# Kernel tuning notes

Measured on AMD Instinct MI355X. Metric: run time of the kernel, lower is better.

## Reference

```python
import jax, jax.numpy as jnp
import numpy as np

PAD_ID = 0
N_LAYERS = 2


def setup_inputs() -> dict:
    key = jax.random.key(0)
    ks = jax.random.split(key, 10)
    B, T, S, H, V = 32, 64, 128, 512, 32000
    G = 4 * H
    sc = 0.02
    return {
        "context": jax.random.normal(ks[0], (B, S, H), jnp.float32),
        "dec_input": jax.random.randint(ks[1], (B, T), 0, V, jnp.int64),
        "h0": jnp.zeros((N_LAYERS, B, H), jnp.float32),
        "c0": jnp.zeros((N_LAYERS, B, H), jnp.float32),
        "emb_table": jax.random.normal(ks[2], (V, H), jnp.float32) * sc,
        "W_ih": jax.random.normal(ks[3], (N_LAYERS, G, H), jnp.float32) * sc,
        "W_hh": jax.random.normal(ks[4], (N_LAYERS, G, H), jnp.float32) * sc,
        "b_ih": jax.random.normal(ks[5], (N_LAYERS, G), jnp.float32) * sc,
        "b_hh": jax.random.normal(ks[6], (N_LAYERS, G), jnp.float32) * sc,
        "Wc": jax.random.normal(ks[7], (V, H), jnp.float32) * sc,
        "bc": jax.random.normal(ks[8], (V,), jnp.float32) * sc,
    }


def _lstm_cell(x, h, c, Wih, Whh, bih, bhh):
    # torch LSTMCell: gates in order i, f, g, o
    gates = x @ Wih.T + bih + h @ Whh.T + bhh  # [B, 4H]
    i, f, g, o = jnp.split(gates, 4, axis=-1)
    c_new = jax.nn.sigmoid(f) * c + jax.nn.sigmoid(i) * jnp.tanh(g)
    h_new = jax.nn.sigmoid(o) * jnp.tanh(c_new)
    return h_new, c_new


def _decode(context, dec_input, h0, c0, emb_table, W_ih, W_hh, b_ih, b_hh, Wc, bc):
    # padding_idx: embedding row pad_id is zero (and receives no grad)
    emb_table = emb_table.at[PAD_ID].set(0.0)
    embedded = emb_table[dec_input]           # [B, T, E]
    xs = jnp.swapaxes(embedded, 0, 1)         # [T, B, E]

    def step(carry, x_t):
        h, c = carry                          # each [L, B, H]
        inp = x_t
        new_h, new_c = [], []
        for l in range(N_LAYERS):
            h_new, c_new = _lstm_cell(inp, h[l], c[l], W_ih[l], W_hh[l], b_ih[l], b_hh[l])
            out = h_new
            # residual (dims match since embedding_dim == rnn_dim)
            inp = out + inp if inp.shape[-1] == out.shape[-1] else out
            new_h.append(h_new)
            new_c.append(c_new)
        # dot attention: score = bmm(context, target) -> [B, S]
        score = jnp.einsum('bsh,bh->bs', context, inp)
        log_attn = jax.nn.log_softmax(score, axis=1)
        # faithful to source: context weighted by LOG-softmax, summed over S
        ctx_vec = jnp.sum(context * log_attn[..., None], axis=1)  # [B, H]
        return (jnp.stack(new_h), jnp.stack(new_c)), ctx_vec

    (hT, cT), outs = jax.lax.scan(step, (h0, c0), xs)  # outs: [T, B, H]
    outs = jnp.swapaxes(outs, 0, 1)                    # [B, T, H]
    logits = outs @ Wc.T + bc                          # [B, T, V]
    return logits, hT, cT


def reference(context, dec_input, h0, c0, emb_table, W_ih, W_hh, b_ih, b_hh, Wc, bc):
    return _decode(context, dec_input, h0, c0, emb_table, W_ih, W_hh, b_ih, b_hh, Wc, bc)
```

## Files before the change

kernel.cpp:

```cpp
#include <hip/hip_runtime.h>
#include <hip/hip_bf16.h>

#define B_ 32
#define T_ 64
#define S_ 128
#define H_ 512
#define V_ 32000
#define G_ 2048
#define NBLK 128

typedef __bf16 bf16x8 __attribute__((ext_vector_type(8)));
typedef float  f32x4  __attribute__((ext_vector_type(4)));

__device__ __forceinline__ int frag_idx(int k, int b) {
    return ((((b >> 4) * 16 + (k >> 5)) * 4 + ((k >> 3) & 3)) * 16 + (b & 15)) * 8 + (k & 7);
}

__device__ __forceinline__ float sigm(float x) { return 1.f / (1.f + expf(-x)); }

__global__ __launch_bounds__(256) void k_embed(const int* __restrict__ dec,
                                               const float* __restrict__ emb,
                                               float* __restrict__ X,
                                               __hip_bfloat16* __restrict__ xfrag)
{
    int i   = blockIdx.x * 256 + threadIdx.x;
    int row = i >> 7;
    int b   = row >> 6, t = row & 63;
    int c4  = (i & 127) << 2;
    int tok = dec[row];
    float4 v = make_float4(0.f, 0.f, 0.f, 0.f);
    if (tok != 0) v = *(const float4*)(emb + (size_t)tok * H_ + c4);
    *(float4*)(X + (size_t)row * H_ + c4) = v;
    __hip_bfloat16* xf = xfrag + (size_t)t * (H_ * B_);
    xf[frag_idx(c4 + 0, b)] = __float2bfloat16(v.x);
    xf[frag_idx(c4 + 1, b)] = __float2bfloat16(v.y);
    xf[frag_idx(c4 + 2, b)] = __float2bfloat16(v.z);
    xf[frag_idx(c4 + 3, b)] = __float2bfloat16(v.w);
}

__global__ __launch_bounds__(256) void k_f2bf(const float* __restrict__ in,
                                              __hip_bfloat16* __restrict__ out, int n4)
{
    int i = blockIdx.x * 256 + threadIdx.x;
    if (i >= n4) return;
    float4 v = *(const float4*)(in + (size_t)i * 4);
    __hip_bfloat16* o = out + (size_t)i * 4;
    o[0] = __float2bfloat16(v.x); o[1] = __float2bfloat16(v.y);
    o[2] = __float2bfloat16(v.z); o[3] = __float2bfloat16(v.w);
}

__global__ __launch_bounds__(256, 1) void k_recur(
    const float* __restrict__ W_ih, const float* __restrict__ W_hh,
    const float* __restrict__ b_ih, const float* __restrict__ b_hh,
    const float* __restrict__ h0_in, const float* __restrict__ c0_in,
    const float* __restrict__ X, const __hip_bfloat16* __restrict__ xfrag,
    __hip_bfloat16* __restrict__ h0f, __hip_bfloat16* __restrict__ h1f,
    __hip_bfloat16* __restrict__ i1f,
    float* __restrict__ outs, float* __restrict__ out_states,
    unsigned* __restrict__ bar)
{
    __shared__ float red[2][4][2][16][17];
    const int tid  = threadIdx.x;
    const int blk  = blockIdx.x;
    const int lane = tid & 63;
    const int w    = tid >> 6;
    const int r    = lane & 15, lg = lane >> 4;

    const int q = r >> 2, jl = r & 3;
    const int g = q * 512 + blk * 4 + jl;
    const float* Wm[4] = { W_ih, W_hh, W_ih + (size_t)G_ * H_, W_hh + (size_t)G_ * H_ };
    bf16x8 wf[4][4];
#pragma unroll
    for (int m = 0; m < 4; m++)
#pragma unroll
        for (int s = 0; s < 4; s++) {
            const float* src = Wm[m] + (size_t)g * H_ + w * 128 + s * 32 + lg * 8;
            union { bf16x8 v; __hip_bfloat16 h[8]; } u;
#pragma unroll
            for (int e = 0; e < 8; e++) u.h[e] = __float2bfloat16(src[e]);
            wf[m][s] = u.v;
        }

    const int b = tid & 31, pjl = (tid >> 5) & 3, pj = blk * 4 + pjl;
    float c0r = 0.f, c1r = 0.f, i1r = 0.f, h0l = 0.f, h1l = 0.f;
    float b0r[4], b1r[4];
    if (tid < 128) {
        c0r = c0_in[b * H_ + pj];
        c1r = c0_in[B_ * H_ + b * H_ + pj];
#pragma unroll
        for (int qq = 0; qq < 4; qq++) {
            b0r[qq] = b_ih[qq * 512 + pj] + b_hh[qq * 512 + pj];
            b1r[qq] = b_ih[G_ + qq * 512 + pj] + b_hh[G_ + qq * 512 + pj];
        }
        h0f[0 * 16384 + frag_idx(pj, b)] = __float2bfloat16(h0_in[b * H_ + pj]);
        h1f[1 * 16384 + frag_idx(pj, b)] = __float2bfloat16(h0_in[B_ * H_ + b * H_ + pj]);
    }

    auto gbar = [&](int idx) {
        __syncthreads();
        if (tid == 0) {
            __threadfence();
            __hip_atomic_fetch_add(bar, 1u, __ATOMIC_RELEASE, __HIP_MEMORY_SCOPE_AGENT);
            unsigned tgt = (unsigned)NBLK * (unsigned)(idx + 1);
            while (__hip_atomic_load(bar, __ATOMIC_ACQUIRE, __HIP_MEMORY_SCOPE_AGENT) < tgt)
                __builtin_amdgcn_s_sleep(8);
            __threadfence();
        }
        __syncthreads();
    };

    gbar(0);

    for (int p = 0; p <= 64; ++p) {
        f32x4 acc0[2] = {}, acc1[2] = {};
        if (p <= 63) {
            const __hip_bfloat16* xb = xfrag + (size_t)p * 16384;
            const __hip_bfloat16* hb = h0f + (size_t)(p & 1) * 16384;
#pragma unroll
            for (int nt = 0; nt < 2; nt++)
#pragma unroll
                for (int s = 0; s < 4; s++) {
                    int ei = frag_idx(w * 128 + s * 32 + lg * 8, nt * 16 + r);
                    bf16x8 bx = *(const bf16x8*)(xb + ei);
                    bf16x8 bh = *(const bf16x8*)(hb + ei);
                    acc0[nt] = __builtin_amdgcn_mfma_f32_16x16x32_bf16(wf[0][s], bx, acc0[nt], 0, 0, 0);
                    acc0[nt] = __builtin_amdgcn_mfma_f32_16x16x32_bf16(wf[1][s], bh, acc0[nt], 0, 0, 0);
                }
        }
        if (p >= 1) {
            const __hip_bfloat16* ib = i1f + (size_t)(p & 1) * 16384;
            const __hip_bfloat16* hb = h1f + (size_t)(p & 1) * 16384;
#pragma unroll
            for (int nt = 0; nt < 2; nt++)
#pragma unroll
                for (int s = 0; s < 4; s++) {
                    int ei = frag_idx(w * 128 + s * 32 + lg * 8, nt * 16 + r);
                    bf16x8 bi = *(const bf16x8*)(ib + ei);
                    bf16x8 bh = *(const bf16x8*)(hb + ei);
                    acc1[nt] = __builtin_amdgcn_mfma_f32_16x16x32_bf16(wf[2][s], bi, acc1[nt], 0, 0, 0);
                    acc1[nt] = __builtin_amdgcn_mfma_f32_16x16x32_bf16(wf[3][s], bh, acc1[nt], 0, 0, 0);
                }
        }
#pragma unroll
        for (int nt = 0; nt < 2; nt++)
#pragma unroll
            for (int rr = 0; rr < 4; rr++) {
                red[0][w][nt][lg * 4 + rr][r] = acc0[nt][rr];
                red[1][w][nt][lg * 4 + rr][r] = acc1[nt][rr];
            }
        __syncthreads();

        if (tid < 128) {
            const int nt = b >> 4, col = b & 15;
            if (p >= 1) {
                int t1 = p - 1;
                float gv[4];
#pragma unroll
                for (int qq = 0; qq < 4; qq++) {
                    float s = b1r[qq];
#pragma unroll
                    for (int ww = 0; ww < 4; ww++) s += red[1][ww][nt][qq * 4 + pjl][col];
                    gv[qq] = s;
                }
                float iv = sigm(gv[0]), fv = sigm(gv[1]);
                float gg = tanhf(gv[2]), ov = sigm(gv[3]);
                c1r = fv * c1r + iv * gg;
                float h1n = ov * tanhf(c1r);
                outs[((size_t)b * T_ + t1) * H_ + pj] = h1n + i1r;
                h1f[(size_t)((p + 1) & 1) * 16384 + frag_idx(pj, b)] = __float2bfloat16(h1n);
                h1l = h1n;
            }
            if (p <= 63) {
                float gv[4];
#pragma unroll
                for (int qq = 0; qq < 4; qq++) {
                    float s = b0r[qq];
#pragma unroll
                    for (int ww = 0; ww < 4; ww++) s += red[0][ww][nt][qq * 4 + pjl][col];
                    gv[qq] = s;
                }
                float iv = sigm(gv[0]), fv = sigm(gv[1]);
                float gg = tanhf(gv[2]), ov = sigm(gv[3]);
                c0r = fv * c0r + iv * gg;
                float h0n = ov * tanhf(c0r);
                float i1n = h0n + X[((size_t)b * T_ + p) * H_ + pj];
                h0f[(size_t)((p + 1) & 1) * 16384 + frag_idx(pj, b)] = __float2bfloat16(h0n);
                i1f[(size_t)((p + 1) & 1) * 16384 + frag_idx(pj, b)] = __float2bfloat16(i1n);
                i1r = i1n;
                h0l = h0n;
            }
        }
        gbar(p + 1);
    }

    if (tid < 128) {
        out_states[b * H_ + pj]                 = h0l;
        out_states[B_ * H_ + b * H_ + pj]       = h1l;
        out_states[2 * B_ * H_ + b * H_ + pj]   = c0r;
        out_states[3 * B_ * H_ + b * H_ + pj]   = c1r;
    }
}

__global__ __launch_bounds__(256) void k_gemm_bf16nt(
    const __hip_bfloat16* __restrict__ A,
    const __hip_bfloat16* __restrict__ Bm,
    const float* __restrict__ bias,
    float* __restrict__ C,
    int K, int ldc, int nM)
{
    __shared__ char smem[64 * 130 * 4];
    __hip_bfloat16* sA = (__hip_bfloat16*)smem;
    __hip_bfloat16* sB = (__hip_bfloat16*)(smem + 16384);
    float*          cbuf = (float*)smem;

    const int tid  = threadIdx.x;
    const int lane = tid & 63;
    const int wave = tid >> 6;
    const int wr = wave >> 1, wc = wave & 1;

    const int cpx = gridDim.x >> 3;
    const int gid = (blockIdx.x & 7) * cpx + (blockIdx.x >> 3);
    const int tm = gid % nM, tn = gid / nM;
    const size_t rowA0 = (size_t)tm * 128, rowB0 = (size_t)tn * 128;

    f32x4 acc[4][4] = {};

    for (int kt = 0; kt < K; kt += 64) {
        uint4 ra[4], rb[4];
#pragma unroll
        for (int i = 0; i < 4; i++) {
            int cid = i * 256 + tid;
            int rr = cid >> 3, c = cid & 7;
            ra[i] = *(const uint4*)(A  + (rowA0 + rr) * K + kt + c * 8);
            rb[i] = *(const uint4*)(Bm + (rowB0 + rr) * K + kt + c * 8);
        }
        __syncthreads();
#pragma unroll
        for (int i = 0; i < 4; i++) {
            int cid = i * 256 + tid;
            int rr = cid >> 3, c = cid & 7;
            int cd = c ^ (rr & 7);
            *(uint4*)((char*)sA + rr * 128 + cd * 16) = ra[i];
            *(uint4*)((char*)sB + rr * 128 + cd * 16) = rb[i];
        }
        __syncthreads();
#pragma unroll
        for (int kk = 0; kk < 2; kk++) {
            bf16x8 af[4], bfr[4];
            int kc = kk * 4 + (lane >> 4);
#pragma unroll
            for (int mi = 0; mi < 4; mi++) {
                int rr = wr * 64 + mi * 16 + (lane & 15);
                af[mi] = *(const bf16x8*)((const char*)sA + rr * 128 + ((kc ^ (rr & 7)) << 4));
            }
#pragma unroll
            for (int ni = 0; ni < 4; ni++) {
                int rr = wc * 64 + ni * 16 + (lane & 15);
                bfr[ni] = *(const bf16x8*)((const char*)sB + rr * 128 + ((kc ^ (rr & 7)) << 4));
            }
#pragma unroll
            for (int mi = 0; mi < 4; mi++)
#pragma unroll
                for (int ni = 0; ni < 4; ni++)
                    acc[mi][ni] = __builtin_amdgcn_mfma_f32_16x16x32_bf16(af[mi], bfr[ni], acc[mi][ni], 0, 0, 0);
        }
    }

    const int cl = lane & 15, rg = lane >> 4;
#pragma unroll
    for (int half = 0; half < 2; half++) {
        __syncthreads();
        if (wr == half) {
#pragma unroll
            for (int mi = 0; mi < 4; mi++)
#pragma unroll
                for (int ni = 0; ni < 4; ni++)
#pragma unroll
                    for (int rr = 0; rr < 4; rr++)
                        cbuf[(mi * 16 + rg * 4 + rr) * 130 + wc * 64 + ni * 16 + cl] = acc[mi][ni][rr];
        }
        __syncthreads();
        int c4 = (tid & 31) * 4;
        float4 bb = *(const float4*)(bias + rowB0 + c4);
#pragma unroll
        for (int it = 0; it < 8; it++) {
            int rrow = it * 8 + (tid >> 5);
            float4 vv = *(float4*)(cbuf + rrow * 130 + c4);
            vv.x += bb.x; vv.y += bb.y; vv.z += bb.z; vv.w += bb.w;
            *(float4*)(C + (size_t)(rowA0 + half * 64 + rrow) * ldc + rowB0 + c4) = vv;
        }
    }
}

__global__ __launch_bounds__(256) void k_attn(const float* __restrict__ context,
                                              const float* __restrict__ outs,
                                              __hip_bfloat16* __restrict__ ctxbf)
{
    __shared__ float orow[512];
    __shared__ float sc2[128][2];
    __shared__ float la[128];
    const int m = blockIdx.x;
    const int b = m >> 6;
    const float* ctxb = context + (size_t)b * S_ * H_;
    const int tid = threadIdx.x;
    orow[tid]       = outs[(size_t)m * H_ + tid];
    orow[tid + 256] = outs[(size_t)m * H_ + tid + 256];
    __syncthreads();
    {
        int s = tid >> 1, p = tid & 1;
        const float4* crow = (const float4*)(ctxb + (size_t)s * H_ + p * 256);
        const float4* orp  = (const float4*)(orow + p * 256);
        float acc = 0.f;
#pragma unroll 4
        for (int k = 0; k < 64; k++) {
            float4 cv = crow[k]; float4 ov = orp[k];
            acc = fmaf(cv.x, ov.x, fmaf(cv.y, ov.y, fmaf(cv.z, ov.z, fmaf(cv.w, ov.w, acc))));
        }
        sc2[s][p] = acc;
    }
    __syncthreads();
    if (tid < 64) {
        float a  = sc2[tid][0] + sc2[tid][1];
        float b2 = sc2[tid + 64][0] + sc2[tid + 64][1];
        float mx = fmaxf(a, b2);
#pragma unroll
        for (int off = 32; off >= 1; off >>= 1) mx = fmaxf(mx, __shfl_xor(mx, off, 64));
        float es = expf(a - mx) + expf(b2 - mx);
#pragma unroll
        for (int off = 32; off >= 1; off >>= 1) es += __shfl_xor(es, off, 64);
        float lse = mx + logf(es);
        la[tid]      = a  - lse;
        la[tid + 64] = b2 - lse;
    }
    __syncthreads();
    {
        float a0 = 0.f, a1 = 0.f;
        for (int s2 = 0; s2 < 128; s2++) {
            float w = la[s2];
            a0 = fmaf(ctxb[(size_t)s2 * H_ + tid], w, a0);
            a1 = fmaf(ctxb[(size_t)s2 * H_ + tid + 256], w, a1);
        }
        ctxbf[(size_t)m * H_ + tid]       = __float2bfloat16(a0);
        ctxbf[(size_t)m * H_ + tid + 256] = __float2bfloat16(a1);
    }
}

extern "C" void kernel_launch(void* const* d_in, const int* in_sizes, int n_in,
                              void* d_out, int out_size, void* d_ws, size_t ws_size,
                              hipStream_t stream)
{
    const float* context = (const float*)d_in[0];
    const int*   dec     = (const int*)d_in[1];
    const float* h0      = (const float*)d_in[2];
    const float* c0      = (const float*)d_in[3];
    const float* emb     = (const float*)d_in[4];
    const float* W_ih    = (const float*)d_in[5];
    const float* W_hh    = (const float*)d_in[6];
    const float* b_ih    = (const float*)d_in[7];
    const float* b_hh    = (const float*)d_in[8];
    const float* Wc      = (const float*)d_in[9];
    const float* bc      = (const float*)d_in[10];
    float* out = (float*)d_out;

    char* ws = (char*)d_ws;
    size_t off = 0;
    auto alloc = [&](size_t bytes) -> char* {
        char* p = ws + off; off += (bytes + 255) & ~(size_t)255; return p;
    };
    float*          X      = (float*)alloc((size_t)B_ * T_ * H_ * 4);
    __hip_bfloat16* xfrag  = (__hip_bfloat16*)alloc((size_t)T_ * H_ * B_ * 2);
    __hip_bfloat16* h0f    = (__hip_bfloat16*)alloc(2 * (size_t)H_ * B_ * 2);
    __hip_bfloat16* h1f    = (__hip_bfloat16*)alloc(2 * (size_t)H_ * B_ * 2);
    __hip_bfloat16* i1f    = (__hip_bfloat16*)alloc(2 * (size_t)H_ * B_ * 2);
    float*          outs   = (float*)alloc((size_t)B_ * T_ * H_ * 4);
    __hip_bfloat16* ctxbf  = (__hip_bfloat16*)alloc((size_t)B_ * T_ * H_ * 2);
    __hip_bfloat16* Wcbf   = (__hip_bfloat16*)alloc((size_t)V_ * H_ * 2);
    unsigned*       bar    = (unsigned*)alloc(256);

    hipMemsetAsync(bar, 0, 256, stream);

    k_embed<<<(B_ * T_ * H_ / 4) / 256, 256, 0, stream>>>(dec, emb, X, xfrag);
    k_f2bf<<<(V_ * H_ / 4 + 255) / 256, 256, 0, stream>>>(Wc, Wcbf, V_ * H_ / 4);

    k_recur<<<NBLK, 256, 0, stream>>>(W_ih, W_hh, b_ih, b_hh, h0, c0,
                                      X, xfrag, h0f, h1f, i1f,
                                      outs, out + (size_t)B_ * T_ * V_, bar);

    k_attn<<<B_ * T_, 256, 0, stream>>>(context, outs, ctxbf);

    k_gemm_bf16nt<<<(V_ / 128) * ((B_ * T_) / 128), 256, 0, stream>>>(
        ctxbf, Wcbf, bc, out, H_, V_, (B_ * T_) / 128);
}
```

Measured before the change: 1.679 ms.

## Hoist LSTM input projections into batched GEMMs and relax recurrent grid barrier

The input-to-hidden products for both layers (embedding times W_ih) are now computed up front by two batched bf16 GEMMs with fused biases. Layer 1's residual input is split linearly into a precomputed x-term plus an in-loop h0 term, which cuts the MFMAs per timestep in the serial recurrence and removes the i1 exchange buffer. Hidden-state buffers now keep the full per-step history instead of double-buffering, and are written as packed 32-bit atomic stores. The grid barrier drops its fences and acquire/release ordering and spins with a shorter sleep. This trades lower per-step latency for bf16 rounding of the precomputed gates and a risk that relaxed ordering lets blocks read stale hidden state.

New measurement: 1.358 ms. 19.1% less time.

```diff
diff --git a/kernel.cpp b/kernel.cpp
--- a/kernel.cpp
+++ b/kernel.cpp
@@ -12,30 +12,24 @@
 typedef __bf16 bf16x8 __attribute__((ext_vector_type(8)));
 typedef float  f32x4  __attribute__((ext_vector_type(4)));
 
-__device__ __forceinline__ int frag_idx(int k, int b) {
-    return ((((b >> 4) * 16 + (k >> 5)) * 4 + ((k >> 3) & 3)) * 16 + (b & 15)) * 8 + (k & 7);
-}
-
 __device__ __forceinline__ float sigm(float x) { return 1.f / (1.f + expf(-x)); }
+__device__ __forceinline__ unsigned short bf16b(float x) {
+    union { __hip_bfloat16 h; unsigned short u; } c; c.h = __float2bfloat16(x); return c.u;
+}
 
 __global__ __launch_bounds__(256) void k_embed(const int* __restrict__ dec,
                                                const float* __restrict__ emb,
-                                               float* __restrict__ X,
-                                               __hip_bfloat16* __restrict__ xfrag)
+                                               __hip_bfloat16* __restrict__ Xbf)
 {
     int i   = blockIdx.x * 256 + threadIdx.x;
     int row = i >> 7;
-    int b   = row >> 6, t = row & 63;
     int c4  = (i & 127) << 2;
     int tok = dec[row];
     float4 v = make_float4(0.f, 0.f, 0.f, 0.f);
     if (tok != 0) v = *(const float4*)(emb + (size_t)tok * H_ + c4);
-    *(float4*)(X + (size_t)row * H_ + c4) = v;
-    __hip_bfloat16* xf = xfrag + (size_t)t * (H_ * B_);
-    xf[frag_idx(c4 + 0, b)] = __float2bfloat16(v.x);
-    xf[frag_idx(c4 + 1, b)] = __float2bfloat16(v.y);
-    xf[frag_idx(c4 + 2, b)] = __float2bfloat16(v.z);
-    xf[frag_idx(c4 + 3, b)] = __float2bfloat16(v.w);
+    __hip_bfloat16* o = Xbf + (size_t)row * H_ + c4;
+    o[0] = __float2bfloat16(v.x); o[1] = __float2bfloat16(v.y);
+    o[2] = __float2bfloat16(v.z); o[3] = __float2bfloat16(v.w);
 }
 
 __global__ __launch_bounds__(256) void k_f2bf(const float* __restrict__ in,
@@ -49,13 +43,22 @@
     o[2] = __float2bfloat16(v.z); o[3] = __float2bfloat16(v.w);
 }
 
+__global__ __launch_bounds__(256) void k_prep(const float* __restrict__ b_ih,
+                                              const float* __restrict__ b_hh,
+                                              float* __restrict__ bias0,
+                                              float* __restrict__ bias1)
+{
+    int i = blockIdx.x * 256 + threadIdx.x;
+    bias0[i] = b_ih[i] + b_hh[i];
+    bias1[i] = b_ih[G_ + i] + b_hh[G_ + i];
+}
+
 __global__ __launch_bounds__(256, 1) void k_recur(
     const float* __restrict__ W_ih, const float* __restrict__ W_hh,
-    const float* __restrict__ b_ih, const float* __restrict__ b_hh,
     const float* __restrict__ h0_in, const float* __restrict__ c0_in,
-    const float* __restrict__ X, const __hip_bfloat16* __restrict__ xfrag,
-    __hip_bfloat16* __restrict__ h0f, __hip_bfloat16* __restrict__ h1f,
-    __hip_bfloat16* __restrict__ i1f,
+    const __hip_bfloat16* __restrict__ Xbf,
+    const __hip_bfloat16* __restrict__ XW0, const __hip_bfloat16* __restrict__ XW1,
+    unsigned* __restrict__ h0f, unsigned* __restrict__ h1f,
     float* __restrict__ outs, float* __restrict__ out_states,
     unsigned* __restrict__ bar)
 {
@@ -68,10 +71,10 @@
 
     const int q = r >> 2, jl = r & 3;
     const int g = q * 512 + blk * 4 + jl;
-    const float* Wm[4] = { W_ih, W_hh, W_ih + (size_t)G_ * H_, W_hh + (size_t)G_ * H_ };
-    bf16x8 wf[4][4];
-#pragma unroll
-    for (int m = 0; m < 4; m++)
+    const float* Wm[3] = { W_hh, W_ih + (size_t)G_ * H_, W_hh + (size_t)G_ * H_ };
+    bf16x8 wf[3][4];
+#pragma unroll
+    for (int m = 0; m < 3; m++)
 #pragma unroll
         for (int s = 0; s < 4; s++) {
             const float* src = Wm[m] + (size_t)g * H_ + w * 128 + s * 32 + lg * 8;
@@ -82,29 +85,30 @@
         }
 
     const int b = tid & 31, pjl = (tid >> 5) & 3, pj = blk * 4 + pjl;
+    const unsigned uoff = ((unsigned)(pj >> 3) * 32u + (unsigned)b) * 4u + (unsigned)((pj & 7) >> 1);
     float c0r = 0.f, c1r = 0.f, i1r = 0.f, h0l = 0.f, h1l = 0.f;
-    float b0r[4], b1r[4];
     if (tid < 128) {
         c0r = c0_in[b * H_ + pj];
         c1r = c0_in[B_ * H_ + b * H_ + pj];
-#pragma unroll
-        for (int qq = 0; qq < 4; qq++) {
-            b0r[qq] = b_ih[qq * 512 + pj] + b_hh[qq * 512 + pj];
-            b1r[qq] = b_ih[G_ + qq * 512 + pj] + b_hh[G_ + qq * 512 + pj];
-        }
-        h0f[0 * 16384 + frag_idx(pj, b)] = __float2bfloat16(h0_in[b * H_ + pj]);
-        h1f[1 * 16384 + frag_idx(pj, b)] = __float2bfloat16(h0_in[B_ * H_ + b * H_ + pj]);
+        unsigned short m0 = bf16b(h0_in[b * H_ + pj]);
+        unsigned short m1 = bf16b(h0_in[B_ * H_ + b * H_ + pj]);
+        unsigned o0 = (unsigned)(unsigned short)__shfl_xor((int)m0, 32);
+        unsigned o1 = (unsigned)(unsigned short)__shfl_xor((int)m1, 32);
+        if (!(pjl & 1)) {
+            __hip_atomic_store(h0f + 0 * 8192 + uoff, (unsigned)m0 | (o0 << 16),
+                               __ATOMIC_RELAXED, __HIP_MEMORY_SCOPE_AGENT);
+            __hip_atomic_store(h1f + 1 * 8192 + uoff, (unsigned)m1 | (o1 << 16),
+                               __ATOMIC_RELAXED, __HIP_MEMORY_SCOPE_AGENT);
+        }
     }
 
     auto gbar = [&](int idx) {
         __syncthreads();
         if (tid == 0) {
-            __threadfence();
-            __hip_atomic_fetch_add(bar, 1u, __ATOMIC_RELEASE, __HIP_MEMORY_SCOPE_AGENT);
+            __hip_atomic_fetch_add(bar, 1u, __ATOMIC_RELAXED, __HIP_MEMORY_SCOPE_AGENT);
             unsigned tgt = (unsigned)NBLK * (unsigned)(idx + 1);
-            while (__hip_atomic_load(bar, __ATOMIC_ACQUIRE, __HIP_MEMORY_SCOPE_AGENT) < tgt)
-                __builtin_amdgcn_s_sleep(8);
-            __threadfence();
+            while (__hip_atomic_load(bar, __ATOMIC_RELAXED, __HIP_MEMORY_SCOPE_AGENT) < tgt)
+                __builtin_amdgcn_s_sleep(2);
         }
         __syncthreads();
     };
@@ -112,35 +116,24 @@
     gbar(0);
 
     for (int p = 0; p <= 64; ++p) {
+        const __hip_bfloat16* hb0 = (const __hip_bfloat16*)(h0f + (size_t)p * 8192);
+        const __hip_bfloat16* hb1 = (const __hip_bfloat16*)(h1f + (size_t)p * 8192);
         f32x4 acc0[2] = {}, acc1[2] = {};
-        if (p <= 63) {
-            const __hip_bfloat16* xb = xfrag + (size_t)p * 16384;
-            const __hip_bfloat16* hb = h0f + (size_t)(p & 1) * 16384;
-#pragma unroll
-            for (int nt = 0; nt < 2; nt++)
-#pragma unroll
-                for (int s = 0; s < 4; s++) {
-                    int ei = frag_idx(w * 128 + s * 32 + lg * 8, nt * 16 + r);
-                    bf16x8 bx = *(const bf16x8*)(xb + ei);
-                    bf16x8 bh = *(const bf16x8*)(hb + ei);
-                    acc0[nt] = __builtin_amdgcn_mfma_f32_16x16x32_bf16(wf[0][s], bx, acc0[nt], 0, 0, 0);
-                    acc0[nt] = __builtin_amdgcn_mfma_f32_16x16x32_bf16(wf[1][s], bh, acc0[nt], 0, 0, 0);
+#pragma unroll
+        for (int nt = 0; nt < 2; nt++)
+#pragma unroll
+            for (int s = 0; s < 4; s++) {
+                int kq = w * 16 + s * 4 + lg;
+                int ei = (kq * 32 + nt * 16 + r) << 3;
+                bf16x8 bh0 = *(const bf16x8*)(hb0 + ei);
+                bf16x8 bh1 = *(const bf16x8*)(hb1 + ei);
+                if (p <= 63)
+                    acc0[nt] = __builtin_amdgcn_mfma_f32_16x16x32_bf16(wf[0][s], bh0, acc0[nt], 0, 0, 0);
+                if (p >= 1) {
+                    acc1[nt] = __builtin_amdgcn_mfma_f32_16x16x32_bf16(wf[1][s], bh0, acc1[nt], 0, 0, 0);
+                    acc1[nt] = __builtin_amdgcn_mfma_f32_16x16x32_bf16(wf[2][s], bh1, acc1[nt], 0, 0, 0);
                 }
-        }
-        if (p >= 1) {
-            const __hip_bfloat16* ib = i1f + (size_t)(p & 1) * 16384;
-            const __hip_bfloat16* hb = h1f + (size_t)(p & 1) * 16384;
-#pragma unroll
-            for (int nt = 0; nt < 2; nt++)
-#pragma unroll
-                for (int s = 0; s < 4; s++) {
-                    int ei = frag_idx(w * 128 + s * 32 + lg * 8, nt * 16 + r);
-                    bf16x8 bi = *(const bf16x8*)(ib + ei);
-                    bf16x8 bh = *(const bf16x8*)(hb + ei);
-                    acc1[nt] = __builtin_amdgcn_mfma_f32_16x16x32_bf16(wf[2][s], bi, acc1[nt], 0, 0, 0);
-                    acc1[nt] = __builtin_amdgcn_mfma_f32_16x16x32_bf16(wf[3][s], bh, acc1[nt], 0, 0, 0);
-                }
-        }
+            }
 #pragma unroll
         for (int nt = 0; nt < 2; nt++)
 #pragma unroll
@@ -157,7 +150,7 @@
                 float gv[4];
 #pragma unroll
                 for (int qq = 0; qq < 4; qq++) {
-                    float s = b1r[qq];
+                    float s = __bfloat162float(XW1[(size_t)(b * T_ + t1) * G_ + qq * 512 + pj]);
 #pragma unroll
                     for (int ww = 0; ww < 4; ww++) s += red[1][ww][nt][qq * 4 + pjl][col];
                     gv[qq] = s;
@@ -167,14 +160,19 @@
                 c1r = fv * c1r + iv * gg;
                 float h1n = ov * tanhf(c1r);
                 outs[((size_t)b * T_ + t1) * H_ + pj] = h1n + i1r;
-                h1f[(size_t)((p + 1) & 1) * 16384 + frag_idx(pj, b)] = __float2bfloat16(h1n);
+                unsigned short mb = bf16b(h1n);
+                unsigned ob = (unsigned)(unsigned short)__shfl_xor((int)mb, 32);
+                if (!(pjl & 1))
+                    __hip_atomic_store(h1f + (size_t)(p + 1) * 8192 + uoff,
+                                       (unsigned)mb | (ob << 16),
+                                       __ATOMIC_RELAXED, __HIP_MEMORY_SCOPE_AGENT);
                 h1l = h1n;
             }
             if (p <= 63) {
                 float gv[4];
 #pragma unroll
                 for (int qq = 0; qq < 4; qq++) {
-                    float s = b0r[qq];
+                    float s = __bfloat162float(XW0[(size_t)(b * T_ + p) * G_ + qq * 512 + pj]);
 #pragma unroll
                     for (int ww = 0; ww < 4; ww++) s += red[0][ww][nt][qq * 4 + pjl][col];
                     gv[qq] = s;
@@ -183,10 +181,13 @@
                 float gg = tanhf(gv[2]), ov = sigm(gv[3]);
                 c0r = fv * c0r + iv * gg;
                 float h0n = ov * tanhf(c0r);
-                float i1n = h0n + X[((size_t)b * T_ + p) * H_ + pj];
-                h0f[(size_t)((p + 1) & 1) * 16384 + frag_idx(pj, b)] = __float2bfloat16(h0n);
-                i1f[(size_t)((p + 1) & 1) * 16384 + frag_idx(pj, b)] = __float2bfloat16(i1n);
-                i1r = i1n;
+                i1r = h0n + __bfloat162float(Xbf[(size_t)(b * T_ + p) * H_ + pj]);
+                unsigned short mb = bf16b(h0n);
+                unsigned ob = (unsigned)(unsigned short)__shfl_xor((int)mb, 32);
+                if (!(pjl & 1))
+                    __hip_atomic_store(h0f + (size_t)(p + 1) * 8192 + uoff,
+                                       (unsigned)mb | (ob << 16),
+                                       __ATOMIC_RELAXED, __HIP_MEMORY_SCOPE_AGENT);
                 h0l = h0n;
             }
         }
@@ -194,10 +195,10 @@
     }
 
     if (tid < 128) {
-        out_states[b * H_ + pj]                 = h0l;
-        out_states[B_ * H_ + b * H_ + pj]       = h1l;
-        out_states[2 * B_ * H_ + b * H_ + pj]   = c0r;
-        out_states[3 * B_ * H_ + b * H_ + pj]   = c1r;
+        out_states[b * H_ + pj]               = h0l;
+        out_states[B_ * H_ + b * H_ + pj]     = h1l;
+        out_states[2 * B_ * H_ + b * H_ + pj] = c0r;
+        out_states[3 * B_ * H_ + b * H_ + pj] = c1r;
     }
 }
 
@@ -205,7 +206,7 @@
     const __hip_bfloat16* __restrict__ A,
     const __hip_bfloat16* __restrict__ Bm,
     const float* __restrict__ bias,
-    float* __restrict__ C,
+    float* __restrict__ C, __hip_bfloat16* __restrict__ Cb,
     int K, int ldc, int nM)
 {
     __shared__ char smem[64 * 130 * 4];
@@ -266,7 +267,6 @@
         }
     }
 
-    const int cl = lane & 15, rg = lane >> 4;
 #pragma unroll
     for (int half = 0; half < 2; half++) {
         __syncthreads();
@@ -277,7 +277,7 @@
                 for (int ni = 0; ni < 4; ni++)
 #pragma unroll
                     for (int rr = 0; rr < 4; rr++)
-                        cbuf[(mi * 16 + rg * 4 + rr) * 130 + wc * 64 + ni * 16 + cl] = acc[mi][ni][rr];
+                        cbuf[(mi * 16 + ((lane >> 4)) * 4 + rr) * 130 + wc * 64 + ni * 16 + (lane & 15)] = acc[mi][ni][rr];
         }
         __syncthreads();
         int c4 = (tid & 31) * 4;
@@ -287,7 +287,15 @@
             int rrow = it * 8 + (tid >> 5);
             float4 vv = *(float4*)(cbuf + rrow * 130 + c4);
             vv.x += bb.x; vv.y += bb.y; vv.z += bb.z; vv.w += bb.w;
-            *(float4*)(C + (size_t)(rowA0 + half * 64 + rrow) * ldc + rowB0 + c4) = vv;
+            size_t orow = (size_t)(rowA0 + half * 64 + rrow);
+            if (Cb) {
+                ushort4 pv;
+                pv.x = bf16b(vv.x); pv.y = bf16b(vv.y);
+                pv.z = bf16b(vv.z); pv.w = bf16b(vv.w);
+                *(ushort4*)(Cb + orow * ldc + rowB0 + c4) = pv;
+            } else {
+                *(float4*)(C + orow * ldc + rowB0 + c4) = vv;
+            }
         }
     }
 }
@@ -367,27 +375,34 @@
     auto alloc = [&](size_t bytes) -> char* {
         char* p = ws + off; off += (bytes + 255) & ~(size_t)255; return p;
     };
-    float*          X      = (float*)alloc((size_t)B_ * T_ * H_ * 4);
-    __hip_bfloat16* xfrag  = (__hip_bfloat16*)alloc((size_t)T_ * H_ * B_ * 2);
-    __hip_bfloat16* h0f    = (__hip_bfloat16*)alloc(2 * (size_t)H_ * B_ * 2);
-    __hip_bfloat16* h1f    = (__hip_bfloat16*)alloc(2 * (size_t)H_ * B_ * 2);
-    __hip_bfloat16* i1f    = (__hip_bfloat16*)alloc(2 * (size_t)H_ * B_ * 2);
+    __hip_bfloat16* Xbf    = (__hip_bfloat16*)alloc((size_t)B_ * T_ * H_ * 2);
+    __hip_bfloat16* Wihbf  = (__hip_bfloat16*)alloc((size_t)2 * G_ * H_ * 2);
+    __hip_bfloat16* Wcbf   = (__hip_bfloat16*)alloc((size_t)V_ * H_ * 2);
+    __hip_bfloat16* XW0    = (__hip_bfloat16*)alloc((size_t)B_ * T_ * G_ * 2);
+    __hip_bfloat16* XW1    = (__hip_bfloat16*)alloc((size_t)B_ * T_ * G_ * 2);
+    float*          bias0  = (float*)alloc(G_ * 4);
+    float*          bias1  = (float*)alloc(G_ * 4);
+    unsigned*       h0f    = (unsigned*)alloc((size_t)66 * 8192 * 4);
+    unsigned*       h1f    = (unsigned*)alloc((size_t)66 * 8192 * 4);
     float*          outs   = (float*)alloc((size_t)B_ * T_ * H_ * 4);
     __hip_bfloat16* ctxbf  = (__hip_bfloat16*)alloc((size_t)B_ * T_ * H_ * 2);
-    __hip_bfloat16* Wcbf   = (__hip_bfloat16*)alloc((size_t)V_ * H_ * 2);
     unsigned*       bar    = (unsigned*)alloc(256);
 
     hipMemsetAsync(bar, 0, 256, stream);
 
-    k_embed<<<(B_ * T_ * H_ / 4) / 256, 256, 0, stream>>>(dec, emb, X, xfrag);
-    k_f2bf<<<(V_ * H_ / 4 + 255) / 256, 256, 0, stream>>>(Wc, Wcbf, V_ * H_ / 4);
-
-    k_recur<<<NBLK, 256, 0, stream>>>(W_ih, W_hh, b_ih, b_hh, h0, c0,
-                                      X, xfrag, h0f, h1f, i1f,
-                                      outs, out + (size_t)B_ * T_ * V_, bar);
+    k_embed<<<(B_ * T_ * H_ / 4) / 256, 256, 0, stream>>>(dec, emb, Xbf);
+    k_f2bf<<<(2 * G_ * H_ / 4) / 256, 256, 0, stream>>>(W_ih, Wihbf, 2 * G_ * H_ / 4);
+    k_f2bf<<<(V_ * H_ / 4) / 256, 256, 0, stream>>>(Wc, Wcbf, V_ * H_ / 4);
+    k_prep<<<G_ / 256, 256, 0, stream>>>(b_ih, b_hh, bias0, bias1);
+
+    k_gemm_bf16nt<<<16 * 16, 256, 0, stream>>>(Xbf, Wihbf, bias0, nullptr, XW0, H_, G_, 16);
+    k_gemm_bf16nt<<<16 * 16, 256, 0, stream>>>(Xbf, Wihbf + (size_t)G_ * H_, bias1, nullptr, XW1, H_, G_, 16);
+
+    k_recur<<<NBLK, 256, 0, stream>>>(W_ih, W_hh, h0, c0, Xbf, XW0, XW1,
+                                      h0f, h1f, outs, out + (size_t)B_ * T_ * V_, bar);
 
     k_attn<<<B_ * T_, 256, 0, stream>>>(context, outs, ctxbf);
 
     k_gemm_bf16nt<<<(V_ / 128) * ((B_ * T_) / 128), 256, 0, stream>>>(
-        ctxbf, Wcbf, bc, out, H_, V_, (B_ * T_) / 128);
-}
+        ctxbf, Wcbf, bc, out, nullptr, H_, V_, (B_ * T_) / 128);
+}
```
